# Kernel tuning notes

Hardware: AMD Instinct MI355X
Metric: run time of the kernel (lower is better)

Reference implementation:

```python
import jax, jax.numpy as jnp
import numpy as np

E, TOPK, H, I, NSH = 8, 2, 2048, 5120, 2
B, S = 2, 1024


def setup_inputs() -> dict:
    key = jax.random.key(0)
    ks = jax.random.split(key, 8)
    sc = 0.02
    return {
        "x": jax.random.normal(ks[0], (B, S, H), dtype=jnp.float32),
        "w_router": jax.random.normal(ks[1], (E, H), dtype=jnp.float32),
        "wg": jax.random.normal(ks[2], (E, I, H), dtype=jnp.float32) * sc,
        "wu": jax.random.normal(ks[3], (E, I, H), dtype=jnp.float32) * sc,
        "wd": jax.random.normal(ks[4], (E, H, I), dtype=jnp.float32) * sc,
        "sg": jax.random.normal(ks[5], (NSH, I, H), dtype=jnp.float32) * sc,
        "su": jax.random.normal(ks[6], (NSH, I, H), dtype=jnp.float32) * sc,
        "sd": jax.random.normal(ks[7], (NSH, H, I), dtype=jnp.float32) * sc,
    }


def reference(x, w_router, wg, wu, wd, sg, su, sd):
    b, s, h = x.shape
    xt = x.reshape(-1, h)  # [T, H]
    T = xt.shape[0]

    # Router: fp32 linear, sigmoid scores, top-k, renormalize
    logits = jnp.einsum('th,eh->te', xt.astype(jnp.float32), w_router.astype(jnp.float32))
    scores = jax.nn.sigmoid(logits)
    topk_w, topk_i = jax.lax.top_k(scores, TOPK)
    topk_w = topk_w / jnp.sum(topk_w, axis=-1, keepdims=True)

    # Dense combine weights [T, E]: zero for non-selected experts
    comb = jnp.zeros((T, E), dtype=xt.dtype)
    comb = comb.at[jnp.arange(T)[:, None], topk_i].add(topk_w.astype(xt.dtype))

    # Routed experts (SwiGLU, no bias): compute all, combine with sparse weights
    gate = jax.nn.silu(jnp.einsum('th,eih->tei', xt, wg))
    up = jnp.einsum('th,eih->tei', xt, wu)
    expert_out = jnp.einsum('tei,ehi->teh', gate * up, wd)
    out = jnp.einsum('te,teh->th', comb, expert_out)

    # Shared experts: applied to every token, summed
    sgate = jax.nn.silu(jnp.einsum('th,jih->tji', xt, sg))
    sup = jnp.einsum('th,jih->tji', xt, su)
    out = out + jnp.einsum('tji,jhi->th', sgate * sup, sd)

    return out.reshape(b, s, h)
```

## Files before the change

### kernel.cpp

```cpp
#include <hip/hip_runtime.h>
#include <stdint.h>


#define E_ 8
#define H_ 2048
#define I_ 5120
#define T_ 2048
#define NSLOT 10

typedef __attribute__((ext_vector_type(4))) float f32x4;
typedef __attribute__((ext_vector_type(8))) __bf16 bf16x8;
typedef __attribute__((ext_vector_type(4))) unsigned int u32x4;
typedef __attribute__((ext_vector_type(2))) unsigned int u32x2;

__device__ __forceinline__ int sw(int r) { return (r ^ (r >> 2)) & 3; }

typedef __attribute__((address_space(1))) const void* gptr1_t;
typedef __attribute__((address_space(3))) void* lptr3_t;
__device__ __forceinline__ void load_lds16(const void* g, void* l) {
  __builtin_amdgcn_global_load_lds((gptr1_t)g, (lptr3_t)l, 16, 0, 0);
}

#define PIPE_SYNC(N)                                                    \
  do {                                                                  \
    asm volatile("s_waitcnt vmcnt(" #N ") lgkmcnt(0)" ::: "memory");    \
    __builtin_amdgcn_sched_barrier(0);                                  \
    __builtin_amdgcn_s_barrier();                                       \
    __builtin_amdgcn_sched_barrier(0);                                  \
  } while (0)

__device__ __forceinline__ unsigned short f2bf(float f) {
  unsigned u = __builtin_bit_cast(unsigned, f);
  u += 0x7FFFu + ((u >> 16) & 1u);
  return (unsigned short)(u >> 16);
}

__device__ __forceinline__ u32x2 cvt4(f32x4 v) {
  unsigned r0, r1;
  asm("v_cvt_pk_bf16_f32 %0, %1, %2" : "=v"(r0) : "v"(v[0]), "v"(v[1]));
  asm("v_cvt_pk_bf16_f32 %0, %1, %2" : "=v"(r1) : "v"(v[2]), "v"(v[3]));
  u32x2 w; w[0] = r0; w[1] = r1;
  return w;
}

__global__ __launch_bounds__(256) void k_castx(const float* __restrict__ x,
                                               unsigned short* __restrict__ xb) {
  const int i = (blockIdx.x * 256 + threadIdx.x) * 8;
  f32x4 a = *(const f32x4*)(x + i);
  f32x4 b = *(const f32x4*)(x + i + 4);
  u32x2 lo = cvt4(a), hi = cvt4(b);
  u32x4 o; o[0] = lo[0]; o[1] = lo[1]; o[2] = hi[0]; o[3] = hi[1];
  *(u32x4*)(xb + i) = o;
}

__global__ __launch_bounds__(64) void k_router(const float* __restrict__ x,
                                               const float* __restrict__ wr,
                                               int* __restrict__ tki,
                                               float* __restrict__ tkw) {
  const int t = blockIdx.x, lane = threadIdx.x;
  const float* xr = x + (size_t)t * H_;
  float lg[E_];
#pragma unroll
  for (int e = 0; e < E_; ++e) {
    const float* w = wr + (size_t)e * H_;
    float acc = 0.f;
    for (int k = lane; k < H_; k += 64) acc += xr[k] * w[k];
#pragma unroll
    for (int off = 32; off > 0; off >>= 1) acc += __shfl_down(acc, off);
    lg[e] = acc;
  }
  if (lane == 0) {
    float sc[E_];
#pragma unroll
    for (int e = 0; e < E_; ++e) sc[e] = 1.f / (1.f + expf(-lg[e]));
    int b0 = 0;
#pragma unroll
    for (int e = 1; e < E_; ++e) if (sc[e] > sc[b0]) b0 = e;
    int b1 = -1;
#pragma unroll
    for (int e = 0; e < E_; ++e) {
      if (e == b0) continue;
      if (b1 < 0 || sc[e] > sc[b1]) b1 = e;
    }
    float s0 = sc[b0], s1 = sc[b1], inv = 1.f / (s0 + s1);
    tki[2 * t] = b0; tki[2 * t + 1] = b1;
    tkw[2 * t] = s0 * inv; tkw[2 * t + 1] = s1 * inv;
  }
}

__global__ __launch_bounds__(64) void k_lists(const int* __restrict__ tki,
                                              const float* __restrict__ tkw,
                                              int* __restrict__ elist,
                                              float* __restrict__ ew,
                                              int* __restrict__ ecnt,
                                              int* __restrict__ ipos) {
  const int s = blockIdx.x, lane = threadIdx.x;
  if (s < E_) {
    int base = 0;
    for (int c = 0; c < T_ / 64; ++c) {
      int t = c * 64 + lane;
      int i0 = tki[2 * t], i1 = tki[2 * t + 1];
      int flag = (i0 == s) ? 1 : ((i1 == s) ? 2 : 0);
      unsigned long long m = __ballot(flag != 0);
      int pre = __popcll(m & ((1ull << lane) - 1ull));
      if (flag) {
        elist[s * T_ + base + pre] = t;
        ew[s * T_ + base + pre] = tkw[2 * t + flag - 1];
        ipos[2 * t + flag - 1] = base + pre;
      }
      base += __popcll(m);
    }
    int padded = (base + 255) & ~255;
    for (int p = base + lane; p < padded; p += 64) { elist[s * T_ + p] = 0; ew[s * T_ + p] = 0.f; }
    if (lane == 0) ecnt[s] = base;
  } else {
    for (int i = lane; i < T_; i += 64) { elist[s * T_ + i] = i; ew[s * T_ + i] = 1.f; }
    if (lane == 0) ecnt[s] = T_;
  }
}

__global__ void k_bases(const int* __restrict__ ecnt, int* __restrict__ sbase) {
  if (threadIdx.x == 0 && blockIdx.x == 0) {
    int b = 0;
    for (int s = 0; s < NSLOT; ++s) { sbase[s] = b; b += (ecnt[s] + 255) & ~255; }
  }
}

__global__ __launch_bounds__(512, 4) void k_gateup(
    const unsigned short* __restrict__ xb,
    const float* __restrict__ wg_all, const float* __restrict__ wu_all,
    const float* __restrict__ sg_all, const float* __restrict__ su_all,
    const int* __restrict__ elist, const float* __restrict__ ew,
    const int* __restrict__ ecnt,
    const int* __restrict__ sbase, unsigned short* __restrict__ h) {
  const int s = blockIdx.z;
  const int cnt = ecnt[s];
  const int r0 = blockIdx.y * 128;
  if (r0 >= cnt) return;
  const int n0 = blockIdx.x * 128;
  const float* gw; const float* uw;
  if (s < E_) { gw = wg_all + (size_t)s * I_ * H_; uw = wu_all + (size_t)s * I_ * H_; }
  else        { gw = sg_all + (size_t)(s - E_) * I_ * H_; uw = su_all + (size_t)(s - E_) * I_ * H_; }
  const int* lst = elist + s * T_;
  const int hrow0 = sbase[s] + r0;

  __shared__ u32x4 sA[2][128 * 4];
  __shared__ u32x4 sG[2][128 * 4];
  __shared__ u32x4 sU[2][128 * 4];

  const int tid = threadIdx.x;
  const int wv = tid >> 6, lane = tid & 63;
  const int wr = wv >> 2, wc = wv & 3;
  const int fr = lane & 15, k8 = lane >> 4;

  const int ar = tid >> 2, ca = tid & 3;
  int li = r0 + ar; if (li >= cnt) li = r0;
  const unsigned short* xp = xb + (size_t)lst[li] * H_ + ca * 8;
  const int br = tid >> 2, cb = tid & 3;
  const float* gp = gw + (size_t)(n0 + br) * H_ + cb * 8;
  const float* up = uw + (size_t)(n0 + br) * H_ + cb * 8;

  u32x4 ra; f32x4 rg0, rg1, ru0, ru1;

  f32x4 accg[4][2], accu[4][2];
#pragma unroll
  for (int m = 0; m < 4; ++m)
#pragma unroll
    for (int n = 0; n < 2; ++n) {
      accg[m][n] = (f32x4){0.f, 0.f, 0.f, 0.f};
      accu[m][n] = (f32x4){0.f, 0.f, 0.f, 0.f};
    }

  auto loadNext = [&]() {
    ra = *(const u32x4*)xp;
    rg0 = *(const f32x4*)gp; rg1 = *(const f32x4*)(gp + 4);
    ru0 = *(const f32x4*)up; ru1 = *(const f32x4*)(up + 4);
    xp += 32; gp += 32; up += 32;
  };
  auto stage = [&](int b) {
    sA[b][ar * 4 + (ca ^ sw(ar))] = ra;
    u32x2 glo = cvt4(rg0), ghi = cvt4(rg1);
    u32x4 gq; gq[0] = glo[0]; gq[1] = glo[1]; gq[2] = ghi[0]; gq[3] = ghi[1];
    sG[b][br * 4 + (cb ^ sw(br))] = gq;
    u32x2 ulo = cvt4(ru0), uhi = cvt4(ru1);
    u32x4 uq; uq[0] = ulo[0]; uq[1] = ulo[1]; uq[2] = uhi[0]; uq[3] = uhi[1];
    sU[b][br * 4 + (cb ^ sw(br))] = uq;
  };
  auto compute = [&](int b) {
    bf16x8 af[4], gf[2], uf[2];
#pragma unroll
    for (int m = 0; m < 4; ++m) {
      int r = wr * 64 + m * 16 + fr;
      af[m] = __builtin_bit_cast(bf16x8, sA[b][r * 4 + (k8 ^ sw(r))]);
    }
#pragma unroll
    for (int n = 0; n < 2; ++n) {
      int r = wc * 32 + n * 16 + fr;
      gf[n] = __builtin_bit_cast(bf16x8, sG[b][r * 4 + (k8 ^ sw(r))]);
      uf[n] = __builtin_bit_cast(bf16x8, sU[b][r * 4 + (k8 ^ sw(r))]);
    }
#pragma unroll
    for (int m = 0; m < 4; ++m)
#pragma unroll
      for (int n = 0; n < 2; ++n) {
        accg[m][n] = __builtin_amdgcn_mfma_f32_16x16x32_bf16(af[m], gf[n], accg[m][n], 0, 0, 0);
        accu[m][n] = __builtin_amdgcn_mfma_f32_16x16x32_bf16(af[m], uf[n], accu[m][n], 0, 0, 0);
      }
  };

  const int KT = H_ / 32;
  loadNext();
  stage(0);
  loadNext();
  __syncthreads();
  int cur = 0;
  for (int kt = 0; kt < KT; ++kt) {
    compute(cur);
    if (kt + 1 < KT) {
      stage(cur ^ 1);
      if (kt + 2 < KT) loadNext();
      __syncthreads();
      cur ^= 1;
    }
  }

#pragma unroll
  for (int m = 0; m < 4; ++m)
#pragma unroll
    for (int r = 0; r < 4; ++r) {
      int rit = wr * 64 + m * 16 + k8 * 4 + r;
      if (r0 + rit < cnt) {
        float wgt = ew[s * T_ + r0 + rit];
        unsigned short* hrow = h + (size_t)(hrow0 + rit) * I_ + n0 + wc * 32;
#pragma unroll
        for (int n = 0; n < 2; ++n) {
          float g = accg[m][n][r], uv = accu[m][n][r];
          float hv = g / (1.f + expf(-g)) * uv * wgt;
          hrow[n * 16 + fr] = f2bf(hv);
        }
      }
    }
}

__global__ __launch_bounds__(512, 4) void k_down(
    const unsigned short* __restrict__ h,
    const float* __restrict__ wd_all, const float* __restrict__ sd_all,
    const int* __restrict__ elist,
    const int* __restrict__ ecnt, const int* __restrict__ sbase,
    float* __restrict__ y, int use_y,
    float* __restrict__ out) {
  const int s = blockIdx.z;
  const int cnt = ecnt[s];
  const int r0 = blockIdx.y * 256;
  if (r0 >= cnt) return;
  const int n0 = blockIdx.x * 128;
  const float* bw = (s < E_) ? wd_all + (size_t)s * H_ * I_
                             : sd_all + (size_t)(s - E_) * H_ * I_;
  const int hrow0 = sbase[s] + r0;

  __shared__ u32x4 sA[3][1024];
  __shared__ u32x4 sB[2][512];

  const int tid = threadIdx.x;
  const int wv = tid >> 6, lane = tid & 63;
  const int wr = wv >> 1, wc = wv & 1;
  const int fr = lane & 15, k8 = lane >> 4;

  const int arow0 = wv * 32 + (lane >> 2);
  const int arow1 = arow0 + 16;
  const unsigned short* aSrc0 =
      h + (size_t)(hrow0 + arow0) * I_ + (((lane & 3) ^ sw(arow0)) * 8);
  const unsigned short* aSrc1 =
      h + (size_t)(hrow0 + arow1) * I_ + (((lane & 3) ^ sw(arow1)) * 8);

  const int brr = tid >> 2, cb = tid & 3;
  const float* bp = bw + (size_t)(n0 + brr) * I_ + cb * 8;
  f32x4 rb0, rb1;

  f32x4 acc[4][4];
#pragma unroll
  for (int m = 0; m < 4; ++m)
#pragma unroll
    for (int n = 0; n < 4; ++n) acc[m][n] = (f32x4){0.f, 0.f, 0.f, 0.f};

  auto dmaA = [&](int b, int kt) {
    load_lds16(aSrc0 + kt * 32, &sA[b][wv * 128]);
    load_lds16(aSrc1 + kt * 32, &sA[b][wv * 128 + 64]);
  };
  auto loadB = [&]() {
    rb0 = *(const f32x4*)bp; rb1 = *(const f32x4*)(bp + 4); bp += 32;
  };
  auto stageB = [&](int b) {
    u32x2 lo = cvt4(rb0), hi = cvt4(rb1);
    u32x4 q; q[0] = lo[0]; q[1] = lo[1]; q[2] = hi[0]; q[3] = hi[1];
    sB[b][brr * 4 + (cb ^ sw(brr))] = q;
  };
  auto compute = [&](int a, int b) {
    bf16x8 af[4], bf[4];
#pragma unroll
    for (int m = 0; m < 4; ++m) {
      int r = wr * 64 + m * 16 + fr;
      af[m] = __builtin_bit_cast(bf16x8, sA[a][r * 4 + (k8 ^ sw(r))]);
    }
#pragma unroll
    for (int n = 0; n < 4; ++n) {
      int r = wc * 64 + n * 16 + fr;
      bf[n] = __builtin_bit_cast(bf16x8, sB[b][r * 4 + (k8 ^ sw(r))]);
    }
#pragma unroll
    for (int m = 0; m < 4; ++m)
#pragma unroll
      for (int n = 0; n < 4; ++n)
        acc[m][n] = __builtin_amdgcn_mfma_f32_16x16x32_bf16(af[m], bf[n], acc[m][n], 0, 0, 0);
  };

  const int KT = I_ / 32;
  loadB();
  dmaA(0, 0);
  stageB(0);
  loadB();
  dmaA(1, 1);
  PIPE_SYNC(4);
  int aCur = 0, bCur = 0;
  for (int kt = 0; kt < KT; ++kt) {
    compute(aCur, bCur);
    if (kt + 1 < KT) {
      stageB(bCur ^ 1);
      if (kt + 2 < KT) {
        int nx = aCur + 2; if (nx >= 3) nx -= 3;
        dmaA(nx, kt + 2);
        loadB();
        PIPE_SYNC(4);
      } else {
        PIPE_SYNC(0);
      }
      aCur = (aCur == 2) ? 0 : aCur + 1;
      bCur ^= 1;
    }
  }

  if (use_y) {
#pragma unroll
    for (int m = 0; m < 4; ++m)
#pragma unroll
      for (int r = 0; r < 4; ++r) {
        int rit = wr * 64 + m * 16 + k8 * 4 + r;
        float* yrow = y + (size_t)(hrow0 + rit) * H_ + n0 + wc * 64 + fr;
#pragma unroll
        for (int n = 0; n < 4; ++n) yrow[n * 16] = acc[m][n][r];
      }
  } else {
    const int* lst = elist + s * T_;
#pragma unroll
    for (int m = 0; m < 4; ++m)
#pragma unroll
      for (int r = 0; r < 4; ++r) {
        int rit = wr * 64 + m * 16 + k8 * 4 + r;
        if (r0 + rit < cnt) {
          int t = lst[r0 + rit];
          float* orow = out + (size_t)t * H_ + n0 + wc * 64 + fr;
#pragma unroll
          for (int n = 0; n < 4; ++n) atomicAdd(orow + n * 16, acc[m][n][r]);
        }
      }
  }
}

__global__ __launch_bounds__(256) void k_combine(
    const float* __restrict__ y, const int* __restrict__ tki,
    const int* __restrict__ ipos, const int* __restrict__ sbase,
    float* __restrict__ out) {
  const int t = blockIdx.x;
  const int c = threadIdx.x * 8;
  const size_t r0 = (size_t)(sbase[tki[2 * t]] + ipos[2 * t]) * H_ + c;
  const size_t r1 = (size_t)(sbase[tki[2 * t + 1]] + ipos[2 * t + 1]) * H_ + c;
  const size_t r2 = (size_t)(sbase[8] + t) * H_ + c;
  const size_t r3 = (size_t)(sbase[9] + t) * H_ + c;
  f32x4 a0 = *(const f32x4*)(y + r0), b0 = *(const f32x4*)(y + r0 + 4);
  f32x4 a1 = *(const f32x4*)(y + r1), b1 = *(const f32x4*)(y + r1 + 4);
  f32x4 a2 = *(const f32x4*)(y + r2), b2 = *(const f32x4*)(y + r2 + 4);
  f32x4 a3 = *(const f32x4*)(y + r3), b3 = *(const f32x4*)(y + r3 + 4);
  f32x4 sa = (a0 + a1) + (a2 + a3);
  f32x4 sb = (b0 + b1) + (b2 + b3);
  float* o = out + (size_t)t * H_ + c;
  *(f32x4*)o = sa;
  *(f32x4*)(o + 4) = sb;
}

extern "C" void kernel_launch(void* const* d_in, const int* in_sizes, int n_in,
                              void* d_out, int out_size, void* d_ws, size_t ws_size,
                              hipStream_t stream) {
  const float* x  = (const float*)d_in[0];
  const float* wr = (const float*)d_in[1];
  const float* wg = (const float*)d_in[2];
  const float* wu = (const float*)d_in[3];
  const float* wd = (const float*)d_in[4];
  const float* sg = (const float*)d_in[5];
  const float* su = (const float*)d_in[6];
  const float* sd = (const float*)d_in[7];
  float* out = (float*)d_out;
  char* ws = (char*)d_ws;

  int*   tki   = (int*)(ws);
  float* tkw   = (float*)(ws + 16384);
  int*   elist = (int*)(ws + 32768);
  float* ew    = (float*)(ws + 114688);
  int*   ecnt  = (int*)(ws + 196608);
  int*   sbase = (int*)(ws + 196864);
  int*   ipos  = (int*)(ws + 197632);
  unsigned short* xb = (unsigned short*)(ws + 262144);
  unsigned short* h  = (unsigned short*)(ws + 262144 + 8388608);
  float* y = (float*)(ws + 262144 + 8388608 + 107479040);
  const size_t ws_need_y = 262144ull + 8388608ull + 107479040ull + 85983232ull;
  const int use_y = (ws_size >= ws_need_y) ? 1 : 0;

  k_castx<<<T_ * H_ / (256 * 8), 256, 0, stream>>>(x, xb);
  k_router<<<T_, 64, 0, stream>>>(x, wr, tki, tkw);
  k_lists<<<NSLOT, 64, 0, stream>>>(tki, tkw, elist, ew, ecnt, ipos);
  k_bases<<<1, 1, 0, stream>>>(ecnt, sbase);
  k_gateup<<<dim3(I_ / 128, T_ / 128, NSLOT), 512, 0, stream>>>(
      xb, wg, wu, sg, su, elist, ew, ecnt, sbase, h);
  if (!use_y) hipMemsetAsync(out, 0, (size_t)T_ * H_ * sizeof(float), stream);
  k_down<<<dim3(H_ / 128, T_ / 256, NSLOT), 512, 0, stream>>>(
      h, wd, sd, elist, ecnt, sbase, y, use_y, out);
  if (use_y)
    k_combine<<<T_, 256, 0, stream>>>(y, tki, ipos, sbase, out);
}
```

Baseline: 1.107 ms.

## Split fused gate/up GEMM into separate kernels with larger row tiles

Replaces the fused gate+up kernel with two kernels: one computes the gate projection and stores it as bf16 in h, the second computes the up projection and applies silu(gate)*up*weight by reading back h. Each kernel uses 256-row by 128-column tiles with a 4x4 MFMA block per wave, halving the number of row tiles that re-read the fp32 weights. The cost is an extra write and read of the intermediate through global memory, an additional launch, and rounding the gate value to bf16 before the activation.

```diff
diff --git a/kernel.cpp b/kernel.cpp
--- a/kernel.cpp
+++ b/kernel.cpp
@@ -33,6 +33,11 @@
   unsigned u = __builtin_bit_cast(unsigned, f);
   u += 0x7FFFu + ((u >> 16) & 1u);
   return (unsigned short)(u >> 16);
+}
+
+__device__ __forceinline__ float bf2f(unsigned short v) {
+  unsigned u = (unsigned)v << 16;
+  return __builtin_bit_cast(float, u);
 }
 
 __device__ __forceinline__ u32x2 cvt4(f32x4 v) {
@@ -126,86 +131,71 @@
   }
 }
 
-__global__ __launch_bounds__(512, 4) void k_gateup(
+__global__ __launch_bounds__(512, 4) void k_gate(
     const unsigned short* __restrict__ xb,
-    const float* __restrict__ wg_all, const float* __restrict__ wu_all,
-    const float* __restrict__ sg_all, const float* __restrict__ su_all,
-    const int* __restrict__ elist, const float* __restrict__ ew,
-    const int* __restrict__ ecnt,
+    const float* __restrict__ wg_all, const float* __restrict__ sg_all,
+    const int* __restrict__ elist, const int* __restrict__ ecnt,
     const int* __restrict__ sbase, unsigned short* __restrict__ h) {
   const int s = blockIdx.z;
   const int cnt = ecnt[s];
-  const int r0 = blockIdx.y * 128;
+  const int r0 = blockIdx.y * 256;
   if (r0 >= cnt) return;
   const int n0 = blockIdx.x * 128;
-  const float* gw; const float* uw;
-  if (s < E_) { gw = wg_all + (size_t)s * I_ * H_; uw = wu_all + (size_t)s * I_ * H_; }
-  else        { gw = sg_all + (size_t)(s - E_) * I_ * H_; uw = su_all + (size_t)(s - E_) * I_ * H_; }
+  const float* bw = (s < E_) ? wg_all + (size_t)s * I_ * H_
+                             : sg_all + (size_t)(s - E_) * I_ * H_;
   const int* lst = elist + s * T_;
   const int hrow0 = sbase[s] + r0;
 
-  __shared__ u32x4 sA[2][128 * 4];
-  __shared__ u32x4 sG[2][128 * 4];
-  __shared__ u32x4 sU[2][128 * 4];
+  __shared__ u32x4 sA[2][1024];
+  __shared__ u32x4 sB[2][512];
 
   const int tid = threadIdx.x;
   const int wv = tid >> 6, lane = tid & 63;
-  const int wr = wv >> 2, wc = wv & 3;
+  const int wr = wv >> 1, wc = wv & 1;
   const int fr = lane & 15, k8 = lane >> 4;
 
-  const int ar = tid >> 2, ca = tid & 3;
+  const int ar = tid >> 1, ca2 = (tid & 1) * 2;
   int li = r0 + ar; if (li >= cnt) li = r0;
-  const unsigned short* xp = xb + (size_t)lst[li] * H_ + ca * 8;
-  const int br = tid >> 2, cb = tid & 3;
-  const float* gp = gw + (size_t)(n0 + br) * H_ + cb * 8;
-  const float* up = uw + (size_t)(n0 + br) * H_ + cb * 8;
-
-  u32x4 ra; f32x4 rg0, rg1, ru0, ru1;
-
-  f32x4 accg[4][2], accu[4][2];
+  const unsigned short* xp = xb + (size_t)lst[li] * H_ + ca2 * 8;
+  const int brr = tid >> 2, cb = tid & 3;
+  const float* bp = bw + (size_t)(n0 + brr) * H_ + cb * 8;
+
+  u32x4 ra0, ra1; f32x4 rb0, rb1;
+
+  f32x4 acc[4][4];
 #pragma unroll
   for (int m = 0; m < 4; ++m)
 #pragma unroll
-    for (int n = 0; n < 2; ++n) {
-      accg[m][n] = (f32x4){0.f, 0.f, 0.f, 0.f};
-      accu[m][n] = (f32x4){0.f, 0.f, 0.f, 0.f};
-    }
+    for (int n = 0; n < 4; ++n) acc[m][n] = (f32x4){0.f, 0.f, 0.f, 0.f};
 
   auto loadNext = [&]() {
-    ra = *(const u32x4*)xp;
-    rg0 = *(const f32x4*)gp; rg1 = *(const f32x4*)(gp + 4);
-    ru0 = *(const f32x4*)up; ru1 = *(const f32x4*)(up + 4);
-    xp += 32; gp += 32; up += 32;
+    ra0 = *(const u32x4*)xp; ra1 = *(const u32x4*)(xp + 8); xp += 32;
+    rb0 = *(const f32x4*)bp; rb1 = *(const f32x4*)(bp + 4); bp += 32;
   };
   auto stage = [&](int b) {
-    sA[b][ar * 4 + (ca ^ sw(ar))] = ra;
-    u32x2 glo = cvt4(rg0), ghi = cvt4(rg1);
-    u32x4 gq; gq[0] = glo[0]; gq[1] = glo[1]; gq[2] = ghi[0]; gq[3] = ghi[1];
-    sG[b][br * 4 + (cb ^ sw(br))] = gq;
-    u32x2 ulo = cvt4(ru0), uhi = cvt4(ru1);
-    u32x4 uq; uq[0] = ulo[0]; uq[1] = ulo[1]; uq[2] = uhi[0]; uq[3] = uhi[1];
-    sU[b][br * 4 + (cb ^ sw(br))] = uq;
+    sA[b][ar * 4 + (ca2 ^ sw(ar))] = ra0;
+    sA[b][ar * 4 + ((ca2 + 1) ^ sw(ar))] = ra1;
+    u32x2 lo = cvt4(rb0), hi = cvt4(rb1);
+    u32x4 q; q[0] = lo[0]; q[1] = lo[1]; q[2] = hi[0]; q[3] = hi[1];
+    sB[b][brr * 4 + (cb ^ sw(brr))] = q;
   };
   auto compute = [&](int b) {
-    bf16x8 af[4], gf[2], uf[2];
+    bf16x8 af[4], bf[4];
 #pragma unroll
     for (int m = 0; m < 4; ++m) {
       int r = wr * 64 + m * 16 + fr;
       af[m] = __builtin_bit_cast(bf16x8, sA[b][r * 4 + (k8 ^ sw(r))]);
     }
 #pragma unroll
-    for (int n = 0; n < 2; ++n) {
-      int r = wc * 32 + n * 16 + fr;
-      gf[n] = __builtin_bit_cast(bf16x8, sG[b][r * 4 + (k8 ^ sw(r))]);
-      uf[n] = __builtin_bit_cast(bf16x8, sU[b][r * 4 + (k8 ^ sw(r))]);
+    for (int n = 0; n < 4; ++n) {
+      int r = wc * 64 + n * 16 + fr;
+      bf[n] = __builtin_bit_cast(bf16x8, sB[b][r * 4 + (k8 ^ sw(r))]);
     }
 #pragma unroll
     for (int m = 0; m < 4; ++m)
 #pragma unroll
-      for (int n = 0; n < 2; ++n) {
-        accg[m][n] = __builtin_amdgcn_mfma_f32_16x16x32_bf16(af[m], gf[n], accg[m][n], 0, 0, 0);
-        accu[m][n] = __builtin_amdgcn_mfma_f32_16x16x32_bf16(af[m], uf[n], accu[m][n], 0, 0, 0);
-      }
+      for (int n = 0; n < 4; ++n)
+        acc[m][n] = __builtin_amdgcn_mfma_f32_16x16x32_bf16(af[m], bf[n], acc[m][n], 0, 0, 0);
   };
 
   const int KT = H_ / 32;
@@ -229,14 +219,109 @@
 #pragma unroll
     for (int r = 0; r < 4; ++r) {
       int rit = wr * 64 + m * 16 + k8 * 4 + r;
+      unsigned short* grow = h + (size_t)(hrow0 + rit) * I_ + n0 + wc * 64 + fr;
+#pragma unroll
+      for (int n = 0; n < 4; ++n) grow[n * 16] = f2bf(acc[m][n][r]);
+    }
+}
+
+__global__ __launch_bounds__(512, 4) void k_up(
+    const unsigned short* __restrict__ xb,
+    const float* __restrict__ wu_all, const float* __restrict__ su_all,
+    const int* __restrict__ elist, const float* __restrict__ ew,
+    const int* __restrict__ ecnt,
+    const int* __restrict__ sbase, unsigned short* __restrict__ h) {
+  const int s = blockIdx.z;
+  const int cnt = ecnt[s];
+  const int r0 = blockIdx.y * 256;
+  if (r0 >= cnt) return;
+  const int n0 = blockIdx.x * 128;
+  const float* bw = (s < E_) ? wu_all + (size_t)s * I_ * H_
+                             : su_all + (size_t)(s - E_) * I_ * H_;
+  const int* lst = elist + s * T_;
+  const int hrow0 = sbase[s] + r0;
+
+  __shared__ u32x4 sA[2][1024];
+  __shared__ u32x4 sB[2][512];
+
+  const int tid = threadIdx.x;
+  const int wv = tid >> 6, lane = tid & 63;
+  const int wr = wv >> 1, wc = wv & 1;
+  const int fr = lane & 15, k8 = lane >> 4;
+
+  const int ar = tid >> 1, ca2 = (tid & 1) * 2;
+  int li = r0 + ar; if (li >= cnt) li = r0;
+  const unsigned short* xp = xb + (size_t)lst[li] * H_ + ca2 * 8;
+  const int brr = tid >> 2, cb = tid & 3;
+  const float* bp = bw + (size_t)(n0 + brr) * H_ + cb * 8;
+
+  u32x4 ra0, ra1; f32x4 rb0, rb1;
+
+  f32x4 acc[4][4];
+#pragma unroll
+  for (int m = 0; m < 4; ++m)
+#pragma unroll
+    for (int n = 0; n < 4; ++n) acc[m][n] = (f32x4){0.f, 0.f, 0.f, 0.f};
+
+  auto loadNext = [&]() {
+    ra0 = *(const u32x4*)xp; ra1 = *(const u32x4*)(xp + 8); xp += 32;
+    rb0 = *(const f32x4*)bp; rb1 = *(const f32x4*)(bp + 4); bp += 32;
+  };
+  auto stage = [&](int b) {
+    sA[b][ar * 4 + (ca2 ^ sw(ar))] = ra0;
+    sA[b][ar * 4 + ((ca2 + 1) ^ sw(ar))] = ra1;
+    u32x2 lo = cvt4(rb0), hi = cvt4(rb1);
+    u32x4 q; q[0] = lo[0]; q[1] = lo[1]; q[2] = hi[0]; q[3] = hi[1];
+    sB[b][brr * 4 + (cb ^ sw(brr))] = q;
+  };
+  auto compute = [&](int b) {
+    bf16x8 af[4], bf[4];
+#pragma unroll
+    for (int m = 0; m < 4; ++m) {
+      int r = wr * 64 + m * 16 + fr;
+      af[m] = __builtin_bit_cast(bf16x8, sA[b][r * 4 + (k8 ^ sw(r))]);
+    }
+#pragma unroll
+    for (int n = 0; n < 4; ++n) {
+      int r = wc * 64 + n * 16 + fr;
+      bf[n] = __builtin_bit_cast(bf16x8, sB[b][r * 4 + (k8 ^ sw(r))]);
+    }
+#pragma unroll
+    for (int m = 0; m < 4; ++m)
+#pragma unroll
+      for (int n = 0; n < 4; ++n)
+        acc[m][n] = __builtin_amdgcn_mfma_f32_16x16x32_bf16(af[m], bf[n], acc[m][n], 0, 0, 0);
+  };
+
+  const int KT = H_ / 32;
+  loadNext();
+  stage(0);
+  loadNext();
+  __syncthreads();
+  int cur = 0;
+  for (int kt = 0; kt < KT; ++kt) {
+    compute(cur);
+    if (kt + 1 < KT) {
+      stage(cur ^ 1);
+      if (kt + 2 < KT) loadNext();
+      __syncthreads();
+      cur ^= 1;
+    }
+  }
+
+#pragma unroll
+  for (int m = 0; m < 4; ++m)
+#pragma unroll
+    for (int r = 0; r < 4; ++r) {
+      int rit = wr * 64 + m * 16 + k8 * 4 + r;
       if (r0 + rit < cnt) {
         float wgt = ew[s * T_ + r0 + rit];
-        unsigned short* hrow = h + (size_t)(hrow0 + rit) * I_ + n0 + wc * 32;
-#pragma unroll
-        for (int n = 0; n < 2; ++n) {
-          float g = accg[m][n][r], uv = accu[m][n][r];
-          float hv = g / (1.f + expf(-g)) * uv * wgt;
-          hrow[n * 16 + fr] = f2bf(hv);
+        unsigned short* hrow = h + (size_t)(hrow0 + rit) * I_ + n0 + wc * 64 + fr;
+#pragma unroll
+        for (int n = 0; n < 4; ++n) {
+          float g = bf2f(hrow[n * 16]);
+          float hv = g / (1.f + expf(-g)) * acc[m][n][r] * wgt;
+          hrow[n * 16] = f2bf(hv);
         }
       }
     }
@@ -418,8 +503,10 @@
   k_router<<<T_, 64, 0, stream>>>(x, wr, tki, tkw);
   k_lists<<<NSLOT, 64, 0, stream>>>(tki, tkw, elist, ew, ecnt, ipos);
   k_bases<<<1, 1, 0, stream>>>(ecnt, sbase);
-  k_gateup<<<dim3(I_ / 128, T_ / 128, NSLOT), 512, 0, stream>>>(
-      xb, wg, wu, sg, su, elist, ew, ecnt, sbase, h);
+  k_gate<<<dim3(I_ / 128, T_ / 256, NSLOT), 512, 0, stream>>>(
+      xb, wg, sg, elist, ecnt, sbase, h);
+  k_up<<<dim3(I_ / 128, T_ / 256, NSLOT), 512, 0, stream>>>(
+      xb, wu, su, elist, ew, ecnt, sbase, h);
   if (!use_y) hipMemsetAsync(out, 0, (size_t)T_ * H_ * sizeof(float), stream);
   k_down<<<dim3(H_ / 128, T_ / 256, NSLOT), 512, 0, stream>>>(
       h, wd, sd, elist, ecnt, sbase, y, use_y, out);
```

Result: slower. 1.182 ms (+6.8%).
